# Optimization experiments

Hardware: AMD Instinct MI355X
Metric: run time of the kernel (lower is better)

The kernel has to match this reference:

```python
import jax, jax.numpy as jnp
import numpy as np

U, I, K = 50000, 30000, 64
D0, D1 = 768, 128
N_INTER = 1_000_000
N_LAYERS = 3
BATCH = 4096
EPS = 1e-12


def setup_inputs() -> dict:
    key = jax.random.key(0)
    k1, k2, k3, k4 = jax.random.split(key, 4)
    rng = np.random.default_rng(0)
    # bidirectional bipartite edges: user u <-> item node (U + i)
    u = rng.integers(0, U, size=N_INTER)
    i = rng.integers(0, I, size=N_INTER) + U
    src = np.concatenate([u, i])
    dst = np.concatenate([i, u])
    edge_index = jnp.asarray(np.stack([src, dst]), dtype=jnp.int32)  # [2, 2*N_INTER]
    return {
        "Gu": jax.random.normal(k1, (U, K), dtype=jnp.float32) * 0.1,
        "F0": jax.random.normal(k2, (I, D0), dtype=jnp.float32),
        "F1": jax.random.normal(k3, (I, D1), dtype=jnp.float32),
        "proj_w": jax.random.normal(k4, (D0 + D1, K), dtype=jnp.float32) * 0.03,
        "proj_b": jnp.zeros((K,), dtype=jnp.float32),
        "edge_index": edge_index,
        "user_idx": jnp.asarray(rng.integers(0, U, size=BATCH), dtype=jnp.int32),
        "item_idx": jnp.asarray(rng.integers(0, I, size=BATCH), dtype=jnp.int32),
    }


def _l2_normalize(x):
    # torch.nn.functional.normalize(p=2, dim=1) with eps clamp
    n = jnp.maximum(jnp.linalg.norm(x, axis=1, keepdims=True), EPS)
    return x / n


def reference(Gu, F0, F1, proj_w, proj_b, edge_index, user_idx, item_idx):
    N = U + I
    # concat aggregation: project concatenated multimodal features, L2-normalize rows
    F_proj = _l2_normalize(jnp.concatenate([F0, F1], axis=-1) @ proj_w + proj_b)
    x = jnp.concatenate([Gu, F_proj], axis=0)  # [N, K]

    src, dst = edge_index[0], edge_index[1]
    # gcn_norm without self-loops (LGConv default): D^{-1/2} A D^{-1/2}
    deg = jax.ops.segment_sum(jnp.ones(src.shape[0], dtype=x.dtype), dst, num_segments=N)
    dinv = jnp.where(deg > 0, jax.lax.rsqrt(jnp.maximum(deg, 1.0)), 0.0)
    norm = dinv[src] * dinv[dst]  # [E]

    layers = [x]
    for _ in range(N_LAYERS):
        msg = layers[-1][src] * norm[:, None]  # [E, K]
        layers.append(jax.ops.segment_sum(msg, dst, num_segments=N))

    all_emb = jnp.mean(jnp.stack(layers, axis=0), axis=0)  # layer-wise mean pooling
    gu, fi = all_emb[:U], all_emb[U:]

    # forward(): batched dot product between selected user/item embeddings
    xui = jnp.sum(gu[user_idx] * fi[item_idx], axis=1)  # [BATCH]
    return xui
```

## Files before the change

### kernel.cpp

```cpp
#include <hip/hip_runtime.h>
#include <hip/hip_bf16.h>

#define NU 50000
#define NI 30000
#define NN 80000
#define KDIM 64
#define DD0 768
#define DD1 128
#define DD 896

#define BROWS 128
#define NB (NN / BROWS)
#define CAPB 5120
#define CAP 96
#define REGION_BYTES 24576
#define ENTS_STRIDE (REGION_BYTES / 4)
#define CHUNK_PAIRS 4096

typedef __attribute__((ext_vector_type(8))) short short8v;
typedef __attribute__((ext_vector_type(4))) short short4v;
typedef __attribute__((ext_vector_type(4))) float float4v;
typedef unsigned short ushort_t;

struct bf16pair { short hi, lo; };

__device__ inline bf16pair f32_split_bf16(float v) {
    __hip_bfloat16 h = __float2bfloat16(v);
    float hf = __bfloat162float(h);
    __hip_bfloat16 l = __float2bfloat16(v - hf);
    bf16pair p;
    p.hi = *reinterpret_cast<short*>(&h);
    p.lo = *reinterpret_cast<short*>(&l);
    return p;
}

__device__ inline float bf16bits_to_f32(ushort_t u) {
    return __uint_as_float(((unsigned int)u) << 16);
}

__device__ inline ushort_t f32_to_bf16_rne(float f) {
    unsigned int u = __float_as_uint(f);
    unsigned int r = (u + 0x7FFFu + ((u >> 16) & 1u)) >> 16;
    return (ushort_t)r;
}

__global__ void wtcvt_kernel(const float* __restrict__ W,
                             short* __restrict__ WTh, short* __restrict__ WTl)
{
    const int i = blockIdx.x * 256 + threadIdx.x;
    if (i < DD * KDIM) {
        const int k = i >> 6, col = i & 63;
        const bf16pair p = f32_split_bf16(W[i]);
        WTh[col * DD + k] = p.hi;
        WTl[col * DD + k] = p.lo;
    }
}

__global__ __launch_bounds__(256) void proj_kernel(
    const float* __restrict__ F0, const float* __restrict__ F1,
    const short* __restrict__ WTh, const short* __restrict__ WTl,
    const float* __restrict__ b, const float* __restrict__ dinv,
    float* __restrict__ Fp, ushort_t* __restrict__ curS)
{
    __shared__ short Ah[64][72];
    __shared__ short Al[64][72];
    __shared__ short Bh[64][72];
    __shared__ short Bl[64][72];

    const int tid  = threadIdx.x;
    const int wv   = tid >> 6;
    const int lane = tid & 63;
    const int lr   = lane & 15;
    const int grp  = lane >> 4;
    const int rowBase = blockIdx.x * 64;

    const int aR[4] = { (0*256+tid) >> 4, (1*256+tid) >> 4,
                        (2*256+tid) >> 4, (3*256+tid) >> 4 };
    const int aK    = (tid & 15) * 4;
    const int bCol[2] = { (0*256+tid) >> 3, (1*256+tid) >> 3 };
    const int bK      = (tid & 7) * 8;

    float4   pA[4];
    short8v  pBh[2], pBl[2];

    auto loadChunk = [&](int c) {
        #pragma unroll
        for (int rep = 0; rep < 4; ++rep) {
            const int r = rowBase + aR[rep];
            float4 v = make_float4(0.f, 0.f, 0.f, 0.f);
            if (r < NI) {
                if (c < 12)
                    v = *(const float4*)&F0[(size_t)r * DD0 + c * 64 + aK];
                else
                    v = *(const float4*)&F1[(size_t)r * DD1 + (c - 12) * 64 + aK];
            }
            pA[rep] = v;
        }
        #pragma unroll
        for (int rep = 0; rep < 2; ++rep) {
            pBh[rep] = *(const short8v*)&WTh[(size_t)bCol[rep] * DD + c * 64 + bK];
            pBl[rep] = *(const short8v*)&WTl[(size_t)bCol[rep] * DD + c * 64 + bK];
        }
    };

    float4v acc[4] = {};

    loadChunk(0);
    for (int c = 0; c < 14; ++c) {
        #pragma unroll
        for (int rep = 0; rep < 4; ++rep) {
            const float4 v = pA[rep];
            const bf16pair p0 = f32_split_bf16(v.x);
            const bf16pair p1 = f32_split_bf16(v.y);
            const bf16pair p2 = f32_split_bf16(v.z);
            const bf16pair p3 = f32_split_bf16(v.w);
            short4v h4, l4;
            h4[0] = p0.hi; h4[1] = p1.hi; h4[2] = p2.hi; h4[3] = p3.hi;
            l4[0] = p0.lo; l4[1] = p1.lo; l4[2] = p2.lo; l4[3] = p3.lo;
            *(short4v*)&Ah[aR[rep]][aK] = h4;
            *(short4v*)&Al[aR[rep]][aK] = l4;
        }
        #pragma unroll
        for (int rep = 0; rep < 2; ++rep) {
            *(short8v*)&Bh[bCol[rep]][bK] = pBh[rep];
            *(short8v*)&Bl[bCol[rep]][bK] = pBl[rep];
        }
        if (c < 13) loadChunk(c + 1);
        __syncthreads();

        #pragma unroll
        for (int ks = 0; ks < 2; ++ks) {
            const int ko = ks * 32 + grp * 8;
            const short8v ah = *(const short8v*)&Ah[wv * 16 + lr][ko];
            const short8v al = *(const short8v*)&Al[wv * 16 + lr][ko];
            #pragma unroll
            for (int nt = 0; nt < 4; ++nt) {
                const short8v bh = *(const short8v*)&Bh[nt * 16 + lr][ko];
                const short8v bl = *(const short8v*)&Bl[nt * 16 + lr][ko];
                acc[nt] = __builtin_amdgcn_mfma_f32_16x16x32_bf16(ah, bh, acc[nt], 0, 0, 0);
                acc[nt] = __builtin_amdgcn_mfma_f32_16x16x32_bf16(ah, bl, acc[nt], 0, 0, 0);
                acc[nt] = __builtin_amdgcn_mfma_f32_16x16x32_bf16(al, bh, acc[nt], 0, 0, 0);
            }
        }
        __syncthreads();
    }

    float bias[4];
    #pragma unroll
    for (int nt = 0; nt < 4; ++nt) bias[nt] = b[nt * 16 + lr];

    float y[4][4];
    float ssp[4];
    #pragma unroll
    for (int i = 0; i < 4; ++i) {
        ssp[i] = 0.f;
        #pragma unroll
        for (int nt = 0; nt < 4; ++nt) {
            y[nt][i] = acc[nt][i] + bias[nt];
            ssp[i] += y[nt][i] * y[nt][i];
        }
    }
    #pragma unroll
    for (int i = 0; i < 4; ++i) {
        float ss = ssp[i];
        ss += __shfl_xor(ss, 1);
        ss += __shfl_xor(ss, 2);
        ss += __shfl_xor(ss, 4);
        ss += __shfl_xor(ss, 8);
        const int r = rowBase + wv * 16 + 4 * grp + i;
        if (r < NI) {
            const float inv = 1.0f / fmaxf(sqrtf(ss), 1e-12f);
            const float dv  = dinv[NU + r];
            #pragma unroll
            for (int nt = 0; nt < 4; ++nt) {
                const float o = y[nt][i] * inv;
                Fp[(size_t)(NU + r) * KDIM + nt * 16 + lr] = o;
                curS[(size_t)(NU + r) * KDIM + nt * 16 + lr] = f32_to_bf16_rne(o * dv);
            }
        }
    }
}

__global__ void userinit_kernel(const float* __restrict__ Gu,
                                const float* __restrict__ dinv,
                                ushort_t* __restrict__ curS)
{
    const int i = blockIdx.x * blockDim.x + threadIdx.x;
    if (i < NU * KDIM / 4) {
        const int row = i >> 4;
        const float dv = dinv[row];
        const float4 g = ((const float4*)Gu)[i];
        short4v s;
        s[0] = (short)f32_to_bf16_rne(g.x * dv);
        s[1] = (short)f32_to_bf16_rne(g.y * dv);
        s[2] = (short)f32_to_bf16_rne(g.z * dv);
        s[3] = (short)f32_to_bf16_rne(g.w * dv);
        *(short4v*)&curS[(size_t)i * 4] = s;
    }
}

__global__ __launch_bounds__(256) void part_kernel(
    const int* __restrict__ src, const int* __restrict__ dst,
    int* __restrict__ bcur, unsigned int* __restrict__ ents, int E2)
{
    __shared__ int bcntL[NB];
    __shared__ int bposL[NB];
    const int tid = threadIdx.x;
    const int pairBase = blockIdx.x * CHUNK_PAIRS;

    for (int i = tid; i < NB; i += 256) bcntL[i] = 0;
    __syncthreads();

    #pragma unroll
    for (int it = 0; it < CHUNK_PAIRS / 256; ++it) {
        const int p = pairBase + it * 256 + tid;
        if (p < E2) {
            const int u  = src[p];
            const int iF = dst[p];
            atomicAdd(&bcntL[iF >> 7], 1);
            atomicAdd(&bcntL[u  >> 7], 1);
        }
    }
    __syncthreads();

    for (int bkt = tid; bkt < NB; bkt += 256) {
        const int c = bcntL[bkt];
        bposL[bkt] = (c > 0) ? atomicAdd(&bcur[bkt], c) : 0;
        bcntL[bkt] = 0;
    }
    __syncthreads();

    #pragma unroll
    for (int it = 0; it < CHUNK_PAIRS / 256; ++it) {
        const int p = pairBase + it * 256 + tid;
        if (p < E2) {
            const int u  = src[p];
            const int iF = dst[p];
            {
                const int bkt = iF >> 7;
                const int k = bposL[bkt] + atomicAdd(&bcntL[bkt], 1);
                if (k < CAPB)
                    ents[(size_t)bkt * ENTS_STRIDE + k] =
                        ((unsigned int)(iF & 127) << 16) | (unsigned int)u;
            }
            {
                const int bkt = u >> 7;
                const int k = bposL[bkt] + atomicAdd(&bcntL[bkt], 1);
                if (k < CAPB)
                    ents[(size_t)bkt * ENTS_STRIDE + k] =
                        ((unsigned int)(u & 127) << 16) | (unsigned int)(iF - NU);
            }
        }
    }
}

__global__ __launch_bounds__(256) void toELL_kernel(
    const int* __restrict__ bcur, unsigned int* __restrict__ ents,
    ushort_t* __restrict__ col,
    int* __restrict__ cnt, float* __restrict__ dinv)
{
    __shared__ unsigned int eL[CAPB];
    __shared__ int curL[BROWS];
    const int bkt = blockIdx.x;
    const int tid = threadIdx.x;

    int n = bcur[bkt]; n = (n < CAPB) ? n : CAPB;
    const unsigned int* ep = ents + (size_t)bkt * ENTS_STRIDE;

    for (int j = tid; j < n; j += 256) eL[j] = ep[j];
    if (tid < BROWS) curL[tid] = 0;
    __syncthreads();

    const size_t rowB = (size_t)bkt * BROWS;
    for (int j = tid; j < n; j += 256) {
        const unsigned int e = eL[j];
        const int dl = (int)(e >> 16);
        const int slot = atomicAdd(&curL[dl], 1);
        if (slot < CAP)
            col[(rowB + dl) * CAP + slot] = (ushort_t)(e & 0xFFFFu);
    }
    __syncthreads();

    if (tid < BROWS) {
        int c = curL[tid];
        c = (c < CAP) ? c : CAP;
        const size_t row = rowB + tid;
        cnt[row]  = c;
        dinv[row] = (c > 0) ? rsqrtf((float)c) : 0.0f;
    }
}

__global__ __launch_bounds__(256) void pull_kernel(
    const ushort_t* __restrict__ curS, ushort_t* __restrict__ nxtS,
    const int* __restrict__ cnt,
    const ushort_t* __restrict__ col,
    const float* __restrict__ dinv,
    int rowStart, int nRows)
{
    const int wid  = (blockIdx.x * blockDim.x + threadIdx.x) >> 6;
    const int lane = threadIdx.x & 63;
    if (wid >= nRows) return;
    const int row = rowStart + wid;
    const int sub = lane & 31;
    const int grp = lane >> 5;

    const ushort_t* cp = col + (size_t)row * CAP;
    const int addB = (row < NU) ? NU : 0;
    const int n = cnt[row];

    float aLo = 0.0f, aHi = 0.0f;
    int j = 0;
    for (; j + 8 <= n; j += 8) {
        int s[4];
        #pragma unroll
        for (int q = 0; q < 4; ++q) s[q] = (int)cp[j + 2 * q + grp] + addB;
        unsigned int v[4];
        #pragma unroll
        for (int q = 0; q < 4; ++q)
            v[q] = *(const unsigned int*)&curS[(size_t)s[q] * KDIM + sub * 2];
        #pragma unroll
        for (int q = 0; q < 4; ++q) {
            aLo += __uint_as_float(v[q] << 16);
            aHi += __uint_as_float(v[q] & 0xFFFF0000u);
        }
    }
    for (; j + 2 <= n; j += 2) {
        const int s = (int)cp[j + grp] + addB;
        const unsigned int v = *(const unsigned int*)&curS[(size_t)s * KDIM + sub * 2];
        aLo += __uint_as_float(v << 16);
        aHi += __uint_as_float(v & 0xFFFF0000u);
    }
    if (j < n && grp == 0) {
        const int s = (int)cp[j] + addB;
        const unsigned int v = *(const unsigned int*)&curS[(size_t)s * KDIM + sub * 2];
        aLo += __uint_as_float(v << 16);
        aHi += __uint_as_float(v & 0xFFFF0000u);
    }

    aLo += __shfl_xor(aLo, 32);
    aHi += __shfl_xor(aHi, 32);

    if (lane < 32) {
        const float dv = dinv[row];
        const float f = dv * dv;
        const unsigned int w = (unsigned int)f32_to_bf16_rne(aLo * f)
                             | ((unsigned int)f32_to_bf16_rne(aHi * f) << 16);
        ((unsigned int*)&nxtS[(size_t)row * KDIM])[sub] = w;
    }
}

__device__ inline float row_acc(int row, float x0, int lane,
                                const ushort_t* __restrict__ S1,
                                const ushort_t* __restrict__ S2,
                                const int* __restrict__ cnt,
                                const ushort_t* __restrict__ col,
                                const float* __restrict__ dinv)
{
    const float dv  = dinv[row];
    const float rdv = (dv > 0.f) ? 1.0f / dv : 0.0f;
    const float s1 = bf16bits_to_f32(S1[(size_t)row * KDIM + lane]);
    const float s2 = bf16bits_to_f32(S2[(size_t)row * KDIM + lane]);

    const ushort_t* cp = col + (size_t)row * CAP;
    const int addB = (row < NU) ? NU : 0;
    const int n = cnt[row];
    float a0 = 0.0f, a1 = 0.0f;
    int j = 0;
    for (; j + 8 <= n; j += 8) {
        int s[8];
        #pragma unroll
        for (int q = 0; q < 8; ++q) s[q] = (int)cp[j + q] + addB;
        float v[8];
        #pragma unroll
        for (int q = 0; q < 8; ++q)
            v[q] = bf16bits_to_f32(S2[(size_t)s[q] * KDIM + lane]);
        a0 += v[0] + v[2] + v[4] + v[6];
        a1 += v[1] + v[3] + v[5] + v[7];
    }
    for (; j < n; ++j)
        a0 += bf16bits_to_f32(S2[(size_t)((int)cp[j] + addB) * KDIM + lane]);

    return x0 + (s1 + s2) * rdv + dv * (a0 + a1);
}

__global__ __launch_bounds__(256) void out_kernel(
    const float* __restrict__ Gu, const float* __restrict__ Fp,
    const ushort_t* __restrict__ S1, const ushort_t* __restrict__ S2,
    const int* __restrict__ cnt, const ushort_t* __restrict__ col,
    const float* __restrict__ dinv,
    const int* __restrict__ uidx, const int* __restrict__ iidx,
    float* __restrict__ out, int B)
{
    const int wid  = (blockIdx.x * blockDim.x + threadIdx.x) >> 6;
    const int lane = threadIdx.x & 63;
    if (wid >= B) return;
    const int u  = uidx[wid];
    const int rI = NU + iidx[wid];

    const float au = row_acc(u,  Gu[(size_t)u  * KDIM + lane], lane,
                             S1, S2, cnt, col, dinv);
    const float ai = row_acc(rI, Fp[(size_t)rI * KDIM + lane], lane,
                             S1, S2, cnt, col, dinv);
    float p = au * ai;
    #pragma unroll
    for (int m = 32; m >= 1; m >>= 1) p += __shfl_xor(p, m);
    if (lane == 0) out[wid] = p * (1.0f / 16.0f);
}

extern "C" void kernel_launch(void* const* d_in, const int* in_sizes, int n_in,
                              void* d_out, int out_size, void* d_ws, size_t ws_size,
                              hipStream_t stream)
{
    const float* Gu = (const float*)d_in[0];
    const float* F0 = (const float*)d_in[1];
    const float* F1 = (const float*)d_in[2];
    const float* W  = (const float*)d_in[3];
    const float* pb = (const float*)d_in[4];
    const int* edge = (const int*)d_in[5];
    const int* uidx = (const int*)d_in[6];
    const int* iidx = (const int*)d_in[7];
    const int E  = in_sizes[5] / 2;
    const int E2 = E / 2;
    const int B = in_sizes[6];
    const int* srcp = edge;
    const int* dstp = edge + E;

    const size_t XE = (size_t)NN * KDIM;
    float*    Fp    = (float*)d_ws;
    ushort_t* curA  = (ushort_t*)(Fp + XE);
    ushort_t* curB  = curA + XE;
    float*    dinv  = (float*)(curB + XE);
    int*      cnt   = (int*)(dinv + NN);
    int*      bcur  = cnt + NN;
    short*    WTh   = (short*)(bcur + NB);
    short*    WTl   = WTh + (size_t)KDIM * DD;
    ushort_t* col   = (ushort_t*)(WTl + (size_t)KDIM * DD);
    unsigned int* ents = (unsigned int*)col;

    (void)hipMemsetAsync(bcur, 0, NB * sizeof(int), stream);
    part_kernel<<<(E2 + CHUNK_PAIRS - 1) / CHUNK_PAIRS, 256, 0, stream>>>(
        srcp, dstp, bcur, ents, E2);
    toELL_kernel<<<NB, 256, 0, stream>>>(bcur, ents, col, cnt, dinv);

    wtcvt_kernel<<<(DD * KDIM + 255) / 256, 256, 0, stream>>>(W, WTh, WTl);

    userinit_kernel<<<(NU * KDIM / 4 + 255) / 256, 256, 0, stream>>>(
        Gu, dinv, curA);
    proj_kernel<<<(NI + 63) / 64, 256, 0, stream>>>(F0, F1, WTh, WTl, pb,
                                                    dinv, Fp, curA);

    const int gridU = (NU * 64 + 255) / 256;
    const int gridI = (NI * 64 + 255) / 256;
    pull_kernel<<<gridU, 256, 0, stream>>>(curA, curB, cnt, col, dinv, 0, NU);
    pull_kernel<<<gridI, 256, 0, stream>>>(curA, curB, cnt, col, dinv, NU, NI);
    pull_kernel<<<gridU, 256, 0, stream>>>(curB, curA, cnt, col, dinv, 0, NU);
    pull_kernel<<<gridI, 256, 0, stream>>>(curB, curA, cnt, col, dinv, NU, NI);

    out_kernel<<<(int)(((size_t)B * 64 + 255) / 256), 256, 0, stream>>>(
        Gu, Fp, curB, curA, cnt, col, dinv, uidx, iidx, (float*)d_out, B);
}
```

Baseline: 193.4 us.

## Halve projection row tile and rework pull kernel to one column per lane

The projection kernel now processes 32 rows per block instead of 64. Each wave computes half the 64 output columns, and the row-norm partial sums are combined through shared memory. This doubles the block count to improve occupancy and load balance across CUs, at the cost of an extra barrier and twice as many reloads of the weight tiles. The pull and output kernels now give each lane one bf16 column, read neighbour indices with a single 16-byte load per 8 edges, keep four accumulators, and make the row id wave-uniform via readfirstlane. This is meant to cut index-load and shuffle overhead in the gather.

```diff
diff --git a/kernel.cpp b/kernel.cpp
--- a/kernel.cpp
+++ b/kernel.cpp
@@ -62,30 +62,32 @@
     const float* __restrict__ b, const float* __restrict__ dinv,
     float* __restrict__ Fp, ushort_t* __restrict__ curS)
 {
-    __shared__ short Ah[64][72];
-    __shared__ short Al[64][72];
+    __shared__ short Ah[32][72];
+    __shared__ short Al[32][72];
     __shared__ short Bh[64][72];
     __shared__ short Bl[64][72];
+    __shared__ float ssL[4][16];
 
     const int tid  = threadIdx.x;
     const int wv   = tid >> 6;
     const int lane = tid & 63;
     const int lr   = lane & 15;
     const int grp  = lane >> 4;
-    const int rowBase = blockIdx.x * 64;
-
-    const int aR[4] = { (0*256+tid) >> 4, (1*256+tid) >> 4,
-                        (2*256+tid) >> 4, (3*256+tid) >> 4 };
+    const int rowBase = blockIdx.x * 32;
+    const int rowGrp  = wv >> 1;
+    const int colHalf = wv & 1;
+
+    const int aR[2] = { (0*256+tid) >> 4, (1*256+tid) >> 4 };
     const int aK    = (tid & 15) * 4;
     const int bCol[2] = { (0*256+tid) >> 3, (1*256+tid) >> 3 };
     const int bK      = (tid & 7) * 8;
 
-    float4   pA[4];
+    float4   pA[2];
     short8v  pBh[2], pBl[2];
 
     auto loadChunk = [&](int c) {
         #pragma unroll
-        for (int rep = 0; rep < 4; ++rep) {
+        for (int rep = 0; rep < 2; ++rep) {
             const int r = rowBase + aR[rep];
             float4 v = make_float4(0.f, 0.f, 0.f, 0.f);
             if (r < NI) {
@@ -103,12 +105,12 @@
         }
     };
 
-    float4v acc[4] = {};
+    float4v acc[2] = {};
 
     loadChunk(0);
     for (int c = 0; c < 14; ++c) {
         #pragma unroll
-        for (int rep = 0; rep < 4; ++rep) {
+        for (int rep = 0; rep < 2; ++rep) {
             const float4 v = pA[rep];
             const bf16pair p0 = f32_split_bf16(v.x);
             const bf16pair p1 = f32_split_bf16(v.y);
@@ -131,12 +133,13 @@
         #pragma unroll
         for (int ks = 0; ks < 2; ++ks) {
             const int ko = ks * 32 + grp * 8;
-            const short8v ah = *(const short8v*)&Ah[wv * 16 + lr][ko];
-            const short8v al = *(const short8v*)&Al[wv * 16 + lr][ko];
+            const short8v ah = *(const short8v*)&Ah[rowGrp * 16 + lr][ko];
+            const short8v al = *(const short8v*)&Al[rowGrp * 16 + lr][ko];
             #pragma unroll
-            for (int nt = 0; nt < 4; ++nt) {
-                const short8v bh = *(const short8v*)&Bh[nt * 16 + lr][ko];
-                const short8v bl = *(const short8v*)&Bl[nt * 16 + lr][ko];
+            for (int nt = 0; nt < 2; ++nt) {
+                const int bc = colHalf * 32 + nt * 16 + lr;
+                const short8v bh = *(const short8v*)&Bh[bc][ko];
+                const short8v bl = *(const short8v*)&Bl[bc][ko];
                 acc[nt] = __builtin_amdgcn_mfma_f32_16x16x32_bf16(ah, bh, acc[nt], 0, 0, 0);
                 acc[nt] = __builtin_amdgcn_mfma_f32_16x16x32_bf16(ah, bl, acc[nt], 0, 0, 0);
                 acc[nt] = __builtin_amdgcn_mfma_f32_16x16x32_bf16(al, bh, acc[nt], 0, 0, 0);
@@ -145,37 +148,40 @@
         __syncthreads();
     }
 
-    float bias[4];
-    #pragma unroll
-    for (int nt = 0; nt < 4; ++nt) bias[nt] = b[nt * 16 + lr];
-
-    float y[4][4];
-    float ssp[4];
+    float bias[2];
+    #pragma unroll
+    for (int nt = 0; nt < 2; ++nt) bias[nt] = b[colHalf * 32 + nt * 16 + lr];
+
+    float y[2][4];
     #pragma unroll
     for (int i = 0; i < 4; ++i) {
-        ssp[i] = 0.f;
-        #pragma unroll
-        for (int nt = 0; nt < 4; ++nt) {
+        float s = 0.f;
+        #pragma unroll
+        for (int nt = 0; nt < 2; ++nt) {
             y[nt][i] = acc[nt][i] + bias[nt];
-            ssp[i] += y[nt][i] * y[nt][i];
-        }
-    }
+            s += y[nt][i] * y[nt][i];
+        }
+        s += __shfl_xor(s, 1);
+        s += __shfl_xor(s, 2);
+        s += __shfl_xor(s, 4);
+        s += __shfl_xor(s, 8);
+        if (lr == 0) ssL[wv][grp * 4 + i] = s;
+    }
+    __syncthreads();
     #pragma unroll
     for (int i = 0; i < 4; ++i) {
-        float ss = ssp[i];
-        ss += __shfl_xor(ss, 1);
-        ss += __shfl_xor(ss, 2);
-        ss += __shfl_xor(ss, 4);
-        ss += __shfl_xor(ss, 8);
-        const int r = rowBase + wv * 16 + 4 * grp + i;
+        const int rl = grp * 4 + i;
+        const float ss = ssL[rowGrp * 2][rl] + ssL[rowGrp * 2 + 1][rl];
+        const int r = rowBase + rowGrp * 16 + rl;
         if (r < NI) {
             const float inv = 1.0f / fmaxf(sqrtf(ss), 1e-12f);
             const float dv  = dinv[NU + r];
             #pragma unroll
-            for (int nt = 0; nt < 4; ++nt) {
+            for (int nt = 0; nt < 2; ++nt) {
                 const float o = y[nt][i] * inv;
-                Fp[(size_t)(NU + r) * KDIM + nt * 16 + lr] = o;
-                curS[(size_t)(NU + r) * KDIM + nt * 16 + lr] = f32_to_bf16_rne(o * dv);
+                const int cc = colHalf * 32 + nt * 16 + lr;
+                Fp[(size_t)(NU + r) * KDIM + cc] = o;
+                curS[(size_t)(NU + r) * KDIM + cc] = f32_to_bf16_rne(o * dv);
             }
         }
     }
@@ -297,56 +303,47 @@
     const float* __restrict__ dinv,
     int rowStart, int nRows)
 {
-    const int wid  = (blockIdx.x * blockDim.x + threadIdx.x) >> 6;
+    const int wid = __builtin_amdgcn_readfirstlane(
+        (int)((blockIdx.x * blockDim.x + threadIdx.x) >> 6));
     const int lane = threadIdx.x & 63;
     if (wid >= nRows) return;
     const int row = rowStart + wid;
-    const int sub = lane & 31;
-    const int grp = lane >> 5;
-
-    const ushort_t* cp = col + (size_t)row * CAP;
+
+    const unsigned int* cpd = (const unsigned int*)(col + (size_t)row * CAP);
     const int addB = (row < NU) ? NU : 0;
     const int n = cnt[row];
 
-    float aLo = 0.0f, aHi = 0.0f;
+    float a0 = 0.f, a1 = 0.f, a2 = 0.f, a3 = 0.f;
     int j = 0;
     for (; j + 8 <= n; j += 8) {
-        int s[4];
-        #pragma unroll
-        for (int q = 0; q < 4; ++q) s[q] = (int)cp[j + 2 * q + grp] + addB;
-        unsigned int v[4];
-        #pragma unroll
-        for (int q = 0; q < 4; ++q)
-            v[q] = *(const unsigned int*)&curS[(size_t)s[q] * KDIM + sub * 2];
-        #pragma unroll
-        for (int q = 0; q < 4; ++q) {
-            aLo += __uint_as_float(v[q] << 16);
-            aHi += __uint_as_float(v[q] & 0xFFFF0000u);
-        }
-    }
-    for (; j + 2 <= n; j += 2) {
-        const int s = (int)cp[j + grp] + addB;
-        const unsigned int v = *(const unsigned int*)&curS[(size_t)s * KDIM + sub * 2];
-        aLo += __uint_as_float(v << 16);
-        aHi += __uint_as_float(v & 0xFFFF0000u);
-    }
-    if (j < n && grp == 0) {
-        const int s = (int)cp[j] + addB;
-        const unsigned int v = *(const unsigned int*)&curS[(size_t)s * KDIM + sub * 2];
-        aLo += __uint_as_float(v << 16);
-        aHi += __uint_as_float(v & 0xFFFF0000u);
-    }
-
-    aLo += __shfl_xor(aLo, 32);
-    aHi += __shfl_xor(aHi, 32);
-
-    if (lane < 32) {
-        const float dv = dinv[row];
-        const float f = dv * dv;
-        const unsigned int w = (unsigned int)f32_to_bf16_rne(aLo * f)
-                             | ((unsigned int)f32_to_bf16_rne(aHi * f) << 16);
-        ((unsigned int*)&nxtS[(size_t)row * KDIM])[sub] = w;
-    }
+        const uint4 cc = *(const uint4*)(cpd + (j >> 1));
+        const int c0 = (int)(cc.x & 0xFFFFu) + addB;
+        const int c1 = (int)(cc.x >> 16)     + addB;
+        const int c2 = (int)(cc.y & 0xFFFFu) + addB;
+        const int c3 = (int)(cc.y >> 16)     + addB;
+        const int c4 = (int)(cc.z & 0xFFFFu) + addB;
+        const int c5 = (int)(cc.z >> 16)     + addB;
+        const int c6 = (int)(cc.w & 0xFFFFu) + addB;
+        const int c7 = (int)(cc.w >> 16)     + addB;
+        const float v0 = bf16bits_to_f32(curS[((size_t)c0 << 6) + lane]);
+        const float v1 = bf16bits_to_f32(curS[((size_t)c1 << 6) + lane]);
+        const float v2 = bf16bits_to_f32(curS[((size_t)c2 << 6) + lane]);
+        const float v3 = bf16bits_to_f32(curS[((size_t)c3 << 6) + lane]);
+        const float v4 = bf16bits_to_f32(curS[((size_t)c4 << 6) + lane]);
+        const float v5 = bf16bits_to_f32(curS[((size_t)c5 << 6) + lane]);
+        const float v6 = bf16bits_to_f32(curS[((size_t)c6 << 6) + lane]);
+        const float v7 = bf16bits_to_f32(curS[((size_t)c7 << 6) + lane]);
+        a0 += v0 + v4; a1 += v1 + v5; a2 += v2 + v6; a3 += v3 + v7;
+    }
+    for (; j < n; ++j) {
+        const unsigned int d = cpd[j >> 1];
+        const int c = (int)((j & 1) ? (d >> 16) : (d & 0xFFFFu)) + addB;
+        a0 += bf16bits_to_f32(curS[((size_t)c << 6) + lane]);
+    }
+
+    const float dv = dinv[row];
+    nxtS[((size_t)row << 6) + lane] =
+        f32_to_bf16_rne(dv * dv * ((a0 + a1) + (a2 + a3)));
 }
 
 __device__ inline float row_acc(int row, float x0, int lane,
@@ -358,29 +355,41 @@
 {
     const float dv  = dinv[row];
     const float rdv = (dv > 0.f) ? 1.0f / dv : 0.0f;
-    const float s1 = bf16bits_to_f32(S1[(size_t)row * KDIM + lane]);
-    const float s2 = bf16bits_to_f32(S2[(size_t)row * KDIM + lane]);
-
-    const ushort_t* cp = col + (size_t)row * CAP;
+    const float s1 = bf16bits_to_f32(S1[((size_t)row << 6) + lane]);
+    const float s2 = bf16bits_to_f32(S2[((size_t)row << 6) + lane]);
+
+    const unsigned int* cpd = (const unsigned int*)(col + (size_t)row * CAP);
     const int addB = (row < NU) ? NU : 0;
     const int n = cnt[row];
-    float a0 = 0.0f, a1 = 0.0f;
+    float a0 = 0.f, a1 = 0.f, a2 = 0.f, a3 = 0.f;
     int j = 0;
     for (; j + 8 <= n; j += 8) {
-        int s[8];
-        #pragma unroll
-        for (int q = 0; q < 8; ++q) s[q] = (int)cp[j + q] + addB;
-        float v[8];
-        #pragma unroll
-        for (int q = 0; q < 8; ++q)
-            v[q] = bf16bits_to_f32(S2[(size_t)s[q] * KDIM + lane]);
-        a0 += v[0] + v[2] + v[4] + v[6];
-        a1 += v[1] + v[3] + v[5] + v[7];
-    }
-    for (; j < n; ++j)
-        a0 += bf16bits_to_f32(S2[(size_t)((int)cp[j] + addB) * KDIM + lane]);
-
-    return x0 + (s1 + s2) * rdv + dv * (a0 + a1);
+        const uint4 cc = *(const uint4*)(cpd + (j >> 1));
+        const int c0 = (int)(cc.x & 0xFFFFu) + addB;
+        const int c1 = (int)(cc.x >> 16)     + addB;
+        const int c2 = (int)(cc.y & 0xFFFFu) + addB;
+        const int c3 = (int)(cc.y >> 16)     + addB;
+        const int c4 = (int)(cc.z & 0xFFFFu) + addB;
+        const int c5 = (int)(cc.z >> 16)     + addB;
+        const int c6 = (int)(cc.w & 0xFFFFu) + addB;
+        const int c7 = (int)(cc.w >> 16)     + addB;
+        const float v0 = bf16bits_to_f32(S2[((size_t)c0 << 6) + lane]);
+        const float v1 = bf16bits_to_f32(S2[((size_t)c1 << 6) + lane]);
+        const float v2 = bf16bits_to_f32(S2[((size_t)c2 << 6) + lane]);
+        const float v3 = bf16bits_to_f32(S2[((size_t)c3 << 6) + lane]);
+        const float v4 = bf16bits_to_f32(S2[((size_t)c4 << 6) + lane]);
+        const float v5 = bf16bits_to_f32(S2[((size_t)c5 << 6) + lane]);
+        const float v6 = bf16bits_to_f32(S2[((size_t)c6 << 6) + lane]);
+        const float v7 = bf16bits_to_f32(S2[((size_t)c7 << 6) + lane]);
+        a0 += v0 + v4; a1 += v1 + v5; a2 += v2 + v6; a3 += v3 + v7;
+    }
+    for (; j < n; ++j) {
+        const unsigned int d = cpd[j >> 1];
+        const int c = (int)((j & 1) ? (d >> 16) : (d & 0xFFFFu)) + addB;
+        a0 += bf16bits_to_f32(S2[((size_t)c << 6) + lane]);
+    }
+
+    return x0 + (s1 + s2) * rdv + dv * ((a0 + a1) + (a2 + a3));
 }
 
 __global__ __launch_bounds__(256) void out_kernel(
@@ -391,15 +400,16 @@
     const int* __restrict__ uidx, const int* __restrict__ iidx,
     float* __restrict__ out, int B)
 {
-    const int wid  = (blockIdx.x * blockDim.x + threadIdx.x) >> 6;
+    const int wid = __builtin_amdgcn_readfirstlane(
+        (int)((blockIdx.x * blockDim.x + threadIdx.x) >> 6));
     const int lane = threadIdx.x & 63;
     if (wid >= B) return;
     const int u  = uidx[wid];
     const int rI = NU + iidx[wid];
 
-    const float au = row_acc(u,  Gu[(size_t)u  * KDIM + lane], lane,
+    const float au = row_acc(u,  Gu[((size_t)u  << 6) + lane], lane,
                              S1, S2, cnt, col, dinv);
-    const float ai = row_acc(rI, Fp[(size_t)rI * KDIM + lane], lane,
+    const float ai = row_acc(rI, Fp[((size_t)rI << 6) + lane], lane,
                              S1, S2, cnt, col, dinv);
     float p = au * ai;
     #pragma unroll
@@ -446,7 +456,7 @@
 
     userinit_kernel<<<(NU * KDIM / 4 + 255) / 256, 256, 0, stream>>>(
         Gu, dinv, curA);
-    proj_kernel<<<(NI + 63) / 64, 256, 0, stream>>>(F0, F1, WTh, WTl, pb,
+    proj_kernel<<<(NI + 31) / 32, 256, 0, stream>>>(F0, F1, WTh, WTl, pb,
                                                     dinv, Fp, curA);
 
     const int gridU = (NU * 64 + 255) / 256;
```

New measurement: 184.6 us. -4.5%, faster.
